# Kernel tuning notes

Measured on AMD Instinct MI355X. Metric: run time of the kernel, lower is better.

Reference implementation:

```python
import jax, jax.numpy as jnp
import numpy as np

NC = 4
X = Y = Z = 64
IMG_SHAPE = (96, 96, 96)
SPAN = 2          # FILTER_SIZE = [5,5,5]
NUM_ITER = 4
DIL = 2           # DILATION = 2.0
SMOOTH_DISTANCE_INIT = 0.3
PRIOR_DISTANCE_INIT = 0.3


def _ind(d):
    # mirrors _get_ind from the torch code
    return (d, 0) if d > 0 else (0, -d)


def _sl(a, b):
    # slice(a, -b) with -0 -> None, mirrors _negative
    return slice(a, -b if b else None)


def _offsets():
    for dx in range(-SPAN, SPAN + 1):
        for dy in range(-SPAN, SPAN + 1):
            for dz in range(-SPAN, SPAN + 1):
                yield dx, dy, dz


def _lin_resize_axis(x, axis, out):
    # 1D linear interpolation matching torch align_corners=True
    n = x.shape[axis]
    if out == n:
        return x
    pos = jnp.arange(out, dtype=x.dtype) * ((n - 1) / (out - 1))
    i0 = jnp.clip(jnp.floor(pos).astype(jnp.int32), 0, n - 1)
    i1 = jnp.clip(i0 + 1, 0, n - 1)
    w = pos - i0.astype(x.dtype)
    shp = [1] * x.ndim
    shp[axis] = out
    w = w.reshape(shp)
    return jnp.take(x, i0, axis=axis) * (1 - w) + jnp.take(x, i1, axis=axis) * w


def _resize3d(x, out_sz):
    # trilinear, align_corners=True, separable over the 3 spatial axes of [b,c,X,Y,Z]
    for ax, o in zip((2, 3, 4), out_sz):
        x = _lin_resize_axis(x, ax, o)
    return x


def _smooth_gaussian(feats):
    # feats: [b, c, X, Y, Z] -> gaussian [b, 5,5,5, X, Y, Z]
    b = feats.shape[0]
    sp = feats.shape[2:]
    g = jnp.zeros((b, 5, 5, 5) + sp, feats.dtype)
    for dx, dy, dz in _offsets():
        dx1, dx2 = _ind(dx); dy1, dy2 = _ind(dy); dz1, dz2 = _ind(dz)
        a = feats[:, :, _sl(dx1, dx2), _sl(dy1, dy2), _sl(dz1, dz2)]
        c = feats[:, :, _sl(dx2, dx1), _sl(dy2, dy1), _sl(dz2, dz1)]
        e = jnp.exp(-0.5 * jnp.sum((a - c) ** 2, axis=1))
        g = g.at[:, dx + SPAN, dy + SPAN, dz + SPAN,
                 _sl(dx2, dx1), _sl(dy2, dy1), _sl(dz2, dz1)].set(e)
    return g


def _prior_gaussian(f1, f2):
    # f1, f2: [b, c, x, y, z] (already downsampled) -> [b, 5,5,5, x, y, z]
    b = f1.shape[0]
    sp = f1.shape[2:]
    g = jnp.zeros((b, 5, 5, 5) + sp, f1.dtype)
    for dx, dy, dz in _offsets():
        dx1, dx2 = _ind(dx); dy1, dy2 = _ind(dy); dz1, dz2 = _ind(dz)
        a = f1[:, :, _sl(dx2, dx1), _sl(dy2, dy1), _sl(dz2, dz1)]
        c = f2[:, :, _sl(dx1, dx2), _sl(dy1, dy2), _sl(dz1, dz2)]
        e = jnp.exp(-0.5 * jnp.sum((a - c) ** 2, axis=1))
        g = g.at[:, dx + SPAN, dy + SPAN, dz + SPAN,
                 _sl(dx2, dx1), _sl(dy2, dy1), _sl(dz2, dz1)].set(e)
    return g


def _message(p, g):
    # p: [b, nc, x, y, z]; g: [b, 5,5,5, x, y, z]
    out = jnp.zeros_like(p)
    for dx, dy, dz in _offsets():
        dx1, dx2 = _ind(dx); dy1, dy2 = _ind(dy); dz1, dz2 = _ind(dz)
        a = p[:, :, _sl(dx1, dx2), _sl(dy1, dy2), _sl(dz1, dz2)]
        w = g[:, None, dx + SPAN, dy + SPAN, dz + SPAN,
              _sl(dx2, dx1), _sl(dy2, dy1), _sl(dz2, dz1)]
        out = out.at[:, :, _sl(dx2, dx1), _sl(dy2, dy1), _sl(dz2, dz1)].add(a * w)
    return out


def setup_inputs() -> dict:
    key = jax.random.key(0)
    ks = jax.random.split(key, 6)
    unary = jax.random.normal(ks[0], (1, NC, X, Y, Z), jnp.float32)
    img = jax.random.normal(ks[1], (1, 2, X, Y, Z), jnp.float32)
    atlas = jax.random.normal(ks[2], (1, 2, X, Y, Z), jnp.float32)
    atlas_label = jax.random.uniform(ks[3], (1, X, Y, Z, NC), jnp.float32)
    patch_start = jax.random.randint(ks[4], (1, 3), 0, 32, jnp.int32)
    return {
        "unary": unary,
        "img": img,
        "atlas": atlas,
        "atlas_label": atlas_label,
        "patch_start": patch_start,
        "smooth_norm": jnp.array([1.0 / SMOOTH_DISTANCE_INIT], jnp.float32),
        "smooth_weight": jnp.ones((NC,), jnp.float32),
        "prior_norm": jnp.array([1.0 / PRIOR_DISTANCE_INIT], jnp.float32),
        "prior_weight": jnp.ones(IMG_SHAPE, jnp.float32),
        "compat_w": jnp.eye(NC, dtype=jnp.float32),
    }


def reference(unary, img, atlas, atlas_label, patch_start,
              smooth_norm, smooth_weight, prior_norm, prior_weight, compat_w):
    b, nc, x, y, z = unary.shape
    ds = (x // DIL, y // DIL, z // DIL)  # floor(in*0.5) == ceil(in/2) for even dims

    # similarity kernels
    sg = _smooth_gaussian(img * smooth_norm)                      # [b,5,5,5,x,y,z]
    f1 = _resize3d(img * prior_norm, ds)
    f2 = _resize3d(atlas * prior_norm, ds)
    pg = _prior_gaussian(f1, f2)                                  # [b,5,5,5,x/2,y/2,z/2]

    # prior message is independent of q_values: compute once
    al = jnp.transpose(atlas_label, (0, 4, 1, 2, 3))              # [b,nc,x,y,z]
    al_ds = _resize3d(al, ds)
    pm = _resize3d(_message(al_ds, pg), (x, y, z))                # [b,nc,x,y,z]
    pw = jax.lax.dynamic_slice(
        prior_weight,
        (patch_start[0, 0], patch_start[0, 1], patch_start[0, 2]),
        (x, y, z))
    prior_term = pw[None, None] * pm

    q = unary
    for _ in range(NUM_ITER):
        p = jax.nn.softmax(q, axis=1)
        sm = _message(p, sg)
        pred = smooth_weight[None, :, None, None, None] * sm + prior_term
        q = unary + jnp.einsum('oc,bcxyz->boxyz', compat_w, pred)  # 1x1x1 compat conv
    return q
```

## Files before the change

### kernel.cpp

```cpp
#include <hip/hip_runtime.h>

#define NN 64
#define N3 (64*64*64)
#define DS 32

#define LOG2E 1.4426950408889634f
#define FSCALE 0.8493218002880191f

typedef _Float16 h2  __attribute__((ext_vector_type(2)));
typedef __fp16   h2f __attribute__((ext_vector_type(2)));

__device__ __forceinline__ float fexp2(float x) { return __builtin_amdgcn_exp2f(x); }

__device__ __forceinline__ h2 u2h(unsigned u) { union { unsigned u; h2 h; } c; c.u = u; return c.h; }
__device__ __forceinline__ unsigned h2u(h2 h) { union { unsigned u; h2 h; } c; c.h = h; return c.u; }
__device__ __forceinline__ h2 pkh(float a, float b) {
    union { h2f a; h2 b; } c; c.a = __builtin_amdgcn_cvt_pkrtz(a, b); return c.b;
}
__device__ __forceinline__ float fdot2(h2 a, h2 b) {
    union { h2 h; h2f f; } ca, cb; ca.h = a; cb.h = b;
    return __builtin_amdgcn_fdot2(ca.f, cb.f, 0.0f, false);
}


#define PMX 6
#define PMY 10
#define PMZ 10
#define SXD 10
#define SYD 14
#define SZD 14

__global__ __launch_bounds__(1024) void k_prior(
    const float* __restrict__ img, const float* __restrict__ atlas,
    const float* __restrict__ alabel, const float* __restrict__ unary,
    const float* __restrict__ pnorm, const float* __restrict__ pweight,
    const int* __restrict__ pstart, const float* __restrict__ compat,
    float4* __restrict__ unary4)
{
    __shared__ __align__(16) uint4 nbS[SXD][SYD][SZD];
    __shared__ __align__(8)  uint2 pmS[PMX][PMY][PMZ];

    const int tid = threadIdx.x;
    const int x0 = blockIdx.z * 8, y0 = blockIdx.y * 16, z0 = blockIdx.x * 16;
    const int cxlo = (x0*31)/63, cylo = (y0*31)/63, czlo = (z0*31)/63;

    const float pnf = pnorm[0] * FSCALE;

    for (int i = tid; i < SXD*SYD*SZD; i += 1024) {
        int lz = i % SZD; int r = i / SZD; int ly = r % SYD; int lx = r / SYD;
        int cx = cxlo - 2 + lx, cy = cylo - 2 + ly, cz = czlo - 2 + lz;
        uint4 v = make_uint4(0u, 0u, 0u, 0u);
        if ((unsigned)cx < DS && (unsigned)cy < DS && (unsigned)cz < DS) {
            const float scale = 63.0f / 31.0f;
            float posx = cx*scale; int a0i = (int)posx; float wx = posx - a0i; int a1i = a0i+1 <= 63 ? a0i+1 : 63;
            float posy = cy*scale; int b0i = (int)posy; float wy = posy - b0i; int b1i = b0i+1 <= 63 ? b0i+1 : 63;
            float posz = cz*scale; int d0i = (int)posz; float wz = posz - d0i; int d1i = d0i+1 <= 63 ? d0i+1 : 63;
            float w000=(1-wx)*(1-wy)*(1-wz), w001=(1-wx)*(1-wy)*wz;
            float w010=(1-wx)*wy*(1-wz),     w011=(1-wx)*wy*wz;
            float w100=wx*(1-wy)*(1-wz),     w101=wx*(1-wy)*wz;
            float w110=wx*wy*(1-wz),         w111=wx*wy*wz;
            int c000=(a0i*NN+b0i)*NN+d0i, c001=(a0i*NN+b0i)*NN+d1i;
            int c010=(a0i*NN+b1i)*NN+d0i, c011=(a0i*NN+b1i)*NN+d1i;
            int c100=(a1i*NN+b0i)*NN+d0i, c101=(a1i*NN+b0i)*NN+d1i;
            int c110=(a1i*NN+b1i)*NN+d0i, c111=(a1i*NN+b1i)*NN+d1i;
            auto tri = [&](const float* p) -> float {
                return p[c000]*w000 + p[c001]*w001 + p[c010]*w010 + p[c011]*w011
                     + p[c100]*w100 + p[c101]*w101 + p[c110]*w110 + p[c111]*w111;
            };
            const float4* lab = (const float4*)alabel;
            float4 l = make_float4(0.f,0.f,0.f,0.f);
            {
                float4 t;
                t = lab[c000]; l.x += w000*t.x; l.y += w000*t.y; l.z += w000*t.z; l.w += w000*t.w;
                t = lab[c001]; l.x += w001*t.x; l.y += w001*t.y; l.z += w001*t.z; l.w += w001*t.w;
                t = lab[c010]; l.x += w010*t.x; l.y += w010*t.y; l.z += w010*t.z; l.w += w010*t.w;
                t = lab[c011]; l.x += w011*t.x; l.y += w011*t.y; l.z += w011*t.z; l.w += w011*t.w;
                t = lab[c100]; l.x += w100*t.x; l.y += w100*t.y; l.z += w100*t.z; l.w += w100*t.w;
                t = lab[c101]; l.x += w101*t.x; l.y += w101*t.y; l.z += w101*t.z; l.w += w101*t.w;
                t = lab[c110]; l.x += w110*t.x; l.y += w110*t.y; l.z += w110*t.z; l.w += w110*t.w;
                t = lab[c111]; l.x += w111*t.x; l.y += w111*t.y; l.z += w111*t.z; l.w += w111*t.w;
            }
            v = make_uint4(h2u(pkh(pnf*tri(atlas), pnf*tri(atlas + N3))),
                           h2u(pkh(l.x, l.y)), h2u(pkh(l.z, l.w)),
                           h2u(pkh(pnf*tri(img), pnf*tri(img + N3))));
        }
        nbS[lx][ly][lz] = v;
    }
    __syncthreads();

    for (int i = tid; i < PMX*PMY*PMZ; i += 1024) {
        int pz = i % PMZ; int r = i / PMZ; int py = r % PMY; int px = r / PMY;
        int cx = cxlo + px, cy = cylo + py, cz = czlo + pz;
        uint2 o = make_uint2(0u, 0u);
        if (cx < DS && cy < DS && cz < DS) {
            h2 ncf = -u2h(nbS[px+2][py+2][pz+2].w);
            float a0=0.f, a1=0.f, a2=0.f, a3=0.f;
            for (int dx = -2; dx <= 2; ++dx) {
                int xx = cx + dx; if ((unsigned)xx >= DS) continue;
                for (int dy = -2; dy <= 2; ++dy) {
                    int yy = cy + dy; if ((unsigned)yy >= DS) continue;
                    #pragma unroll
                    for (int dz = -2; dz <= 2; ++dz) {
                        int zz = cz + dz; if ((unsigned)zz >= DS) continue;
                        uint4 v = nbS[px+2+dx][py+2+dy][pz+2+dz];
                        h2 d = u2h(v.x) + ncf;
                        float w = fexp2(-fdot2(d, d));
                        h2 l01 = u2h(v.y), l23 = u2h(v.z);
                        a0 += w*(float)l01.x; a1 += w*(float)l01.y;
                        a2 += w*(float)l23.x; a3 += w*(float)l23.y;
                    }
                }
            }
            o = make_uint2(h2u(pkh(a0, a1)), h2u(pkh(a2, a3)));
        }
        pmS[px][py][pz] = o;
    }
    __syncthreads();

    const int ps0 = pstart[0], ps1 = pstart[1], ps2 = pstart[2];
    float cw[16];
    #pragma unroll
    for (int k = 0; k < 16; ++k) cw[k] = compat[k];
    const float S13 = 31.0f / 63.0f;

    for (int i = tid; i < 8*16*16; i += 1024) {
        int fz = i & 15, fy = (i >> 4) & 15, fx = i >> 8;
        int gx = x0 + fx, gy = y0 + fy, gz = z0 + fz;
        float posx = gx*S13; int xc0 = (int)posx; float wx = posx - xc0; int xc1 = xc0 < 31 ? xc0+1 : 31;
        float posy = gy*S13; int yc0 = (int)posy; float wy = posy - yc0; int yc1 = yc0 < 31 ? yc0+1 : 31;
        float posz = gz*S13; int zc0 = (int)posz; float wz = posz - zc0; int zc1 = zc0 < 31 ? zc0+1 : 31;
        int lx0 = xc0-cxlo, lx1 = xc1-cxlo;
        int ly0 = yc0-cylo, ly1 = yc1-cylo;
        int lz0 = zc0-czlo, lz1 = zc1-czlo;

        auto up = [&](uint2 u) -> float4 {
            h2 a = u2h(u.x), b = u2h(u.y);
            return make_float4((float)a.x, (float)a.y, (float)b.x, (float)b.y);
        };
        float4 p000 = up(pmS[lx0][ly0][lz0]), p001 = up(pmS[lx0][ly0][lz1]);
        float4 p010 = up(pmS[lx0][ly1][lz0]), p011 = up(pmS[lx0][ly1][lz1]);
        float4 p100 = up(pmS[lx1][ly0][lz0]), p101 = up(pmS[lx1][ly0][lz1]);
        float4 p110 = up(pmS[lx1][ly1][lz0]), p111 = up(pmS[lx1][ly1][lz1]);
        float w000=(1-wx)*(1-wy)*(1-wz), w001=(1-wx)*(1-wy)*wz;
        float w010=(1-wx)*wy*(1-wz),     w011=(1-wx)*wy*wz;
        float w100=wx*(1-wy)*(1-wz),     w101=wx*(1-wy)*wz;
        float w110=wx*wy*(1-wz),         w111=wx*wy*wz;
        float pw = pweight[(ps0+gx)*96*96 + (ps1+gy)*96 + (ps2+gz)];
        float pr0 = pw*(w000*p000.x + w001*p001.x + w010*p010.x + w011*p011.x + w100*p100.x + w101*p101.x + w110*p110.x + w111*p111.x);
        float pr1 = pw*(w000*p000.y + w001*p001.y + w010*p010.y + w011*p011.y + w100*p100.y + w101*p101.y + w110*p110.y + w111*p111.y);
        float pr2 = pw*(w000*p000.z + w001*p001.z + w010*p010.z + w011*p011.z + w100*p100.z + w101*p101.z + w110*p110.z + w111*p111.z);
        float pr3 = pw*(w000*p000.w + w001*p001.w + w010*p010.w + w011*p011.w + w100*p100.w + w101*p101.w + w110*p110.w + w111*p111.w);

        int g = (gx*NN + gy)*NN + gz;
        float4 q;
        q.x = unary[g]      + cw[0]*pr0  + cw[1]*pr1  + cw[2]*pr2  + cw[3]*pr3;
        q.y = unary[g+N3]   + cw[4]*pr0  + cw[5]*pr1  + cw[6]*pr2  + cw[7]*pr3;
        q.z = unary[g+2*N3] + cw[8]*pr0  + cw[9]*pr1  + cw[10]*pr2 + cw[11]*pr3;
        q.w = unary[g+3*N3] + cw[12]*pr0 + cw[13]*pr1 + cw[14]*pr2 + cw[15]*pr3;
        unary4[g] = q;
    }
}


#define TXD 8
#define TYD 8
#define TZD 8
#define RZ 4
#define HX 12
#define HY 12
#define HZ 12
#define PZ 14
#define PZF 20

template<bool QV_IN, bool QV_OUT>
__global__ __launch_bounds__(1024, 8) void k_iter(
    const float* __restrict__ qin,
    const float4* __restrict__ unary4,
    const float* __restrict__ img,
    const float* __restrict__ snorm,
    const float* __restrict__ sweight,
    const float* __restrict__ compat,
    float* __restrict__ qout)
{
    __shared__ __align__(16) uint2    pS[HX][HY][PZ];
    __shared__ __align__(16) unsigned fS[HX][HY][PZF];
    __shared__ __align__(16) uint4    accA[7][TXD*TYD*2];
    __shared__ __align__(16) uint4    accB[7][TXD*TYD*2];

    const int tzg = threadIdx.x, ty = threadIdx.y;
    const int tx = threadIdx.z & 7, s = threadIdx.z >> 3;
    const int x0b = blockIdx.z * TXD, y0b = blockIdx.y * TYD, z0b = blockIdx.x * TZD;
    const int tid = threadIdx.x + 2*threadIdx.y + 16*threadIdx.z;
    const float sc = snorm[0] * FSCALE;

    #pragma unroll
    for (int rr = 0; rr < 2; ++rr) {
        int i = tid + rr*1024;
        if (i < HX*HY*HZ) {
            int lz = i % HZ; int r = i / HZ;
            int ly = r % HY; int lx = r / HY;
            int gx = x0b + lx - 2, gy = y0b + ly - 2, gz = z0b + lz - 2;
            uint2 pu = make_uint2(0u, 0u);
            unsigned fu = 0u;
            if ((unsigned)gx < NN && (unsigned)gy < NN && (unsigned)gz < NN) {
                int g = (gx*NN + gy)*NN + gz;
                float q0, q1, q2, q3;
                if (QV_IN) {
                    float4 qv = reinterpret_cast<const float4*>(qin)[g];
                    q0 = qv.x; q1 = qv.y; q2 = qv.z; q3 = qv.w;
                } else {
                    q0 = qin[g]; q1 = qin[g+N3]; q2 = qin[g+2*N3]; q3 = qin[g+3*N3];
                }
                float m = fmaxf(fmaxf(q0,q1), fmaxf(q2,q3));
                float e0 = fexp2((q0-m)*LOG2E);
                float e1 = fexp2((q1-m)*LOG2E);
                float e2 = fexp2((q2-m)*LOG2E);
                float e3 = fexp2((q3-m)*LOG2E);
                float inv = 1.0f/(e0+e1+e2+e3);
                pu = make_uint2(h2u(pkh(e0*inv, e1*inv)), h2u(pkh(e2*inv, e3*inv)));
                fu = h2u(pkh(img[g]*sc, img[g+N3]*sc));
            }
            pS[lx][ly][lz] = pu;
            fS[lx][ly][lz] = fu;
        }
    }
    __syncthreads();

    const int tz0 = tzg * RZ;

    h2 ncf[RZ];
    #pragma unroll
    for (int rz = 0; rz < RZ; ++rz) ncf[rz] = -u2h(fS[tx+2][ty+2][tz0+2+rz]);

    h2 a01[RZ], a23[RZ];
    #pragma unroll
    for (int rz = 0; rz < RZ; ++rz) { a01[rz] = (h2)0; a23[rz] = (h2)0; }

    #pragma unroll
    for (int pp = 0; pp < 4; ++pp) {
        int p = (7 - s) + 8*pp;
        if (p < 25) {
            int dx = p / 5, dy = p - 5*dx;
            const uint4* pv = reinterpret_cast<const uint4*>(&pS[tx+dx][ty+dy][tz0]);
            uint4 qa = pv[0], qb = pv[1], qc = pv[2], qd = pv[3];
            const uint4* fv = reinterpret_cast<const uint4*>(&fS[tx+dx][ty+dy][tz0]);
            uint4 fa = fv[0], fb = fv[1];

            unsigned fz[8]  = { fa.x, fa.y, fa.z, fa.w, fb.x, fb.y, fb.z, fb.w };
            unsigned p01[8] = { qa.x, qa.z, qb.x, qb.z, qc.x, qc.z, qd.x, qd.z };
            unsigned p23[8] = { qa.y, qa.w, qb.y, qb.w, qc.y, qc.w, qd.y, qd.w };

            #pragma unroll
            for (int rz = 0; rz < RZ; ++rz) {
                #pragma unroll
                for (int dz = 0; dz < 5; ++dz) {
                    int k = rz + dz;
                    h2 d = u2h(fz[k]) + ncf[rz];
                    float w = fexp2(-fdot2(d, d));
                    h2 w2 = pkh(w, w);
                    a01[rz] = w2 * u2h(p01[k]) + a01[rz];
                    a23[rz] = w2 * u2h(p23[k]) + a23[rz];
                }
            }
        }
    }

    const int pid = (tx*TYD + ty)*2 + tzg;
    if (s != 0) {
        accA[s-1][pid] = make_uint4(h2u(a01[0]), h2u(a01[1]), h2u(a01[2]), h2u(a01[3]));
        accB[s-1][pid] = make_uint4(h2u(a23[0]), h2u(a23[1]), h2u(a23[2]), h2u(a23[3]));
    }
    __syncthreads();

    if (s == 0) {
        #pragma unroll
        for (int j = 0; j < 7; ++j) {
            uint4 va = accA[j][pid];
            a01[0] += u2h(va.x); a01[1] += u2h(va.y); a01[2] += u2h(va.z); a01[3] += u2h(va.w);
            uint4 vb = accB[j][pid];
            a23[0] += u2h(vb.x); a23[1] += u2h(vb.y); a23[2] += u2h(vb.z); a23[3] += u2h(vb.w);
        }

        const int gx = x0b + tx, gy = y0b + ty;
        const int g = (gx*NN + gy)*NN + z0b + tz0;
        const float sw0 = sweight[0], sw1 = sweight[1], sw2 = sweight[2], sw3 = sweight[3];
        float cw[16];
        #pragma unroll
        for (int k = 0; k < 16; ++k) cw[k] = compat[k];

        float r[4][RZ];
        #pragma unroll
        for (int rz = 0; rz < RZ; ++rz) {
            float4 u4 = unary4[g + rz];
            float p0 = sw0*(float)a01[rz].x, p1 = sw1*(float)a01[rz].y;
            float p2 = sw2*(float)a23[rz].x, p3 = sw3*(float)a23[rz].y;
            r[0][rz] = u4.x + cw[0]*p0  + cw[1]*p1  + cw[2]*p2  + cw[3]*p3;
            r[1][rz] = u4.y + cw[4]*p0  + cw[5]*p1  + cw[6]*p2  + cw[7]*p3;
            r[2][rz] = u4.z + cw[8]*p0  + cw[9]*p1  + cw[10]*p2 + cw[11]*p3;
            r[3][rz] = u4.w + cw[12]*p0 + cw[13]*p1 + cw[14]*p2 + cw[15]*p3;
        }

        if (QV_OUT) {
            float4* qo = reinterpret_cast<float4*>(qout);
            #pragma unroll
            for (int rz = 0; rz < RZ; ++rz)
                qo[g + rz] = make_float4(r[0][rz], r[1][rz], r[2][rz], r[3][rz]);
        } else {
            #pragma unroll
            for (int o = 0; o < 4; ++o)
                *(float4*)(qout + o*N3 + g) = make_float4(r[o][0], r[o][1], r[o][2], r[o][3]);
        }
    }
}


extern "C" void kernel_launch(void* const* d_in, const int* in_sizes, int n_in,
                              void* d_out, int out_size, void* d_ws, size_t ws_size,
                              hipStream_t stream)
{
    const float* unary   = (const float*)d_in[0];
    const float* img     = (const float*)d_in[1];
    const float* atlas   = (const float*)d_in[2];
    const float* alabel  = (const float*)d_in[3];
    const int*   pstart  = (const int*)d_in[4];
    const float* snorm   = (const float*)d_in[5];
    const float* sweight = (const float*)d_in[6];
    const float* pnorm   = (const float*)d_in[7];
    const float* pweight = (const float*)d_in[8];
    const float* compat  = (const float*)d_in[9];
    float* out = (float*)d_out;
    float* ws  = (float*)d_ws;

    float4* unary4 = (float4*)ws;
    float*  qA     = ws + 4*N3;
    float*  qB     = ws + 8*N3;

    {
        dim3 pgrid(4, 4, 8), pblock(1024);
        k_prior<<<pgrid, pblock, 0, stream>>>(img, atlas, alabel, unary, pnorm,
                                              pweight, pstart, compat, unary4);
    }

    dim3 grid(NN/TZD, NN/TYD, NN/TXD), block(2, 8, 64);
    k_iter<false,true><<<grid, block, 0, stream>>>(unary, unary4, img, snorm, sweight, compat, qA);
    k_iter<true, true><<<grid, block, 0, stream>>>(qA,    unary4, img, snorm, sweight, compat, qB);
    k_iter<true, true><<<grid, block, 0, stream>>>(qB,    unary4, img, snorm, sweight, compat, qA);
    k_iter<true,false><<<grid, block, 0, stream>>>(qA,    unary4, img, snorm, sweight, compat, out);
}
```

Before: 93.25 us.

## Store fp16 softmax probabilities between iterations and precompute packed image features

Each iteration kernel now applies softmax in its epilogue and writes packed fp16 probabilities, so the next iteration loads 8 bytes per voxel instead of 16 bytes of fp32 logits and recomputes no exps in its halo. The packed, scaled image features are computed once in the prior kernel and reused by all four iterations. The thread mapping changes to 4 z-groups of 2 outputs each with 4 neighbour-splits instead of 8, which shrinks the shared reduction buffers and cuts register pressure. Unary and weight loads are hoisted ahead of the barrier. The cost is fp16 rounding on the probabilities carried between iterations, and the first launch passes the same buffer as its pin and pout, although FIRST never reads pin.

```diff
diff --git a/kernel.cpp b/kernel.cpp
--- a/kernel.cpp
+++ b/kernel.cpp
@@ -33,9 +33,10 @@
 __global__ __launch_bounds__(1024) void k_prior(
     const float* __restrict__ img, const float* __restrict__ atlas,
     const float* __restrict__ alabel, const float* __restrict__ unary,
-    const float* __restrict__ pnorm, const float* __restrict__ pweight,
-    const int* __restrict__ pstart, const float* __restrict__ compat,
-    float4* __restrict__ unary4)
+    const float* __restrict__ pnorm, const float* __restrict__ snorm,
+    const float* __restrict__ pweight, const int* __restrict__ pstart,
+    const float* __restrict__ compat,
+    float4* __restrict__ unary4, unsigned* __restrict__ fpk)
 {
     __shared__ __align__(16) uint4 nbS[SXD][SYD][SZD];
     __shared__ __align__(8)  uint2 pmS[PMX][PMY][PMZ];
@@ -45,6 +46,13 @@
     const int cxlo = (x0*31)/63, cylo = (y0*31)/63, czlo = (z0*31)/63;
 
     const float pnf = pnorm[0] * FSCALE;
+    const float sc  = snorm[0] * FSCALE;
+
+    for (int i = tid; i < 8*16*16; i += 1024) {
+        int fz = i & 15, fy = (i >> 4) & 15, fx = i >> 8;
+        int g = ((x0+fx)*NN + (y0+fy))*NN + (z0+fz);
+        fpk[g] = h2u(pkh(img[g]*sc, img[g+N3]*sc));
+    }
 
     for (int i = tid; i < SXD*SYD*SZD; i += 1024) {
         int lz = i % SZD; int r = i / SZD; int ly = r % SYD; int lx = r / SYD;
@@ -165,33 +173,32 @@
 #define TXD 8
 #define TYD 8
 #define TZD 8
-#define RZ 4
+#define TZR 4
+#define RZ 2
 #define HX 12
 #define HY 12
 #define HZ 12
 #define PZ 14
-#define PZF 20
-
-template<bool QV_IN, bool QV_OUT>
+
+template<bool FIRST, bool LAST>
 __global__ __launch_bounds__(1024, 8) void k_iter(
     const float* __restrict__ qin,
+    const uint2* __restrict__ pin,
+    const unsigned* __restrict__ fpk,
     const float4* __restrict__ unary4,
-    const float* __restrict__ img,
-    const float* __restrict__ snorm,
     const float* __restrict__ sweight,
     const float* __restrict__ compat,
+    uint2* __restrict__ pout,
     float* __restrict__ qout)
 {
     __shared__ __align__(16) uint2    pS[HX][HY][PZ];
-    __shared__ __align__(16) unsigned fS[HX][HY][PZF];
-    __shared__ __align__(16) uint4    accA[7][TXD*TYD*2];
-    __shared__ __align__(16) uint4    accB[7][TXD*TYD*2];
+    __shared__ __align__(8)  unsigned fS[HX][HY][PZ];
+    __shared__ __align__(16) uint4    accS[3][TXD*TYD*TZR];
 
     const int tzg = threadIdx.x, ty = threadIdx.y;
     const int tx = threadIdx.z & 7, s = threadIdx.z >> 3;
     const int x0b = blockIdx.z * TXD, y0b = blockIdx.y * TYD, z0b = blockIdx.x * TZD;
-    const int tid = threadIdx.x + 2*threadIdx.y + 16*threadIdx.z;
-    const float sc = snorm[0] * FSCALE;
+    const int tid = threadIdx.x + TZR*threadIdx.y + (TZR*TYD)*threadIdx.z;
 
     #pragma unroll
     for (int rr = 0; rr < 2; ++rr) {
@@ -204,111 +211,126 @@
             unsigned fu = 0u;
             if ((unsigned)gx < NN && (unsigned)gy < NN && (unsigned)gz < NN) {
                 int g = (gx*NN + gy)*NN + gz;
-                float q0, q1, q2, q3;
-                if (QV_IN) {
-                    float4 qv = reinterpret_cast<const float4*>(qin)[g];
-                    q0 = qv.x; q1 = qv.y; q2 = qv.z; q3 = qv.w;
+                fu = fpk[g];
+                if (FIRST) {
+                    float q0 = qin[g], q1 = qin[g+N3], q2 = qin[g+2*N3], q3 = qin[g+3*N3];
+                    float m = fmaxf(fmaxf(q0,q1), fmaxf(q2,q3));
+                    float e0 = fexp2((q0-m)*LOG2E);
+                    float e1 = fexp2((q1-m)*LOG2E);
+                    float e2 = fexp2((q2-m)*LOG2E);
+                    float e3 = fexp2((q3-m)*LOG2E);
+                    float inv = 1.0f/(e0+e1+e2+e3);
+                    pu = make_uint2(h2u(pkh(e0*inv, e1*inv)), h2u(pkh(e2*inv, e3*inv)));
                 } else {
-                    q0 = qin[g]; q1 = qin[g+N3]; q2 = qin[g+2*N3]; q3 = qin[g+3*N3];
+                    pu = pin[g];
                 }
-                float m = fmaxf(fmaxf(q0,q1), fmaxf(q2,q3));
-                float e0 = fexp2((q0-m)*LOG2E);
-                float e1 = fexp2((q1-m)*LOG2E);
-                float e2 = fexp2((q2-m)*LOG2E);
-                float e3 = fexp2((q3-m)*LOG2E);
-                float inv = 1.0f/(e0+e1+e2+e3);
-                pu = make_uint2(h2u(pkh(e0*inv, e1*inv)), h2u(pkh(e2*inv, e3*inv)));
-                fu = h2u(pkh(img[g]*sc, img[g+N3]*sc));
             }
             pS[lx][ly][lz] = pu;
             fS[lx][ly][lz] = fu;
         }
     }
+
+    const int tz0 = tzg * RZ;
+    const int gx = x0b + tx, gy = y0b + ty;
+    const int g = (gx*NN + gy)*NN + z0b + tz0;
+
+    float4 u40, u41;
+    float sw0, sw1, sw2, sw3;
+    float cw[16];
+    if (s == 0) {
+        u40 = unary4[g]; u41 = unary4[g+1];
+        sw0 = sweight[0]; sw1 = sweight[1]; sw2 = sweight[2]; sw3 = sweight[3];
+        #pragma unroll
+        for (int k = 0; k < 16; ++k) cw[k] = compat[k];
+    }
+
     __syncthreads();
 
-    const int tz0 = tzg * RZ;
-
-    h2 ncf[RZ];
+    const h2 ncf0 = -u2h(fS[tx+2][ty+2][tz0+2]);
+    const h2 ncf1 = -u2h(fS[tx+2][ty+2][tz0+3]);
+
+    h2 a01_0 = (h2)0, a23_0 = (h2)0, a01_1 = (h2)0, a23_1 = (h2)0;
+
     #pragma unroll
-    for (int rz = 0; rz < RZ; ++rz) ncf[rz] = -u2h(fS[tx+2][ty+2][tz0+2+rz]);
-
-    h2 a01[RZ], a23[RZ];
-    #pragma unroll
-    for (int rz = 0; rz < RZ; ++rz) { a01[rz] = (h2)0; a23[rz] = (h2)0; }
-
-    #pragma unroll
-    for (int pp = 0; pp < 4; ++pp) {
-        int p = (7 - s) + 8*pp;
+    for (int pp = 0; pp < 7; ++pp) {
+        int p = (3 - s) + 4*pp;
         if (p < 25) {
             int dx = p / 5, dy = p - 5*dx;
             const uint4* pv = reinterpret_cast<const uint4*>(&pS[tx+dx][ty+dy][tz0]);
-            uint4 qa = pv[0], qb = pv[1], qc = pv[2], qd = pv[3];
-            const uint4* fv = reinterpret_cast<const uint4*>(&fS[tx+dx][ty+dy][tz0]);
-            uint4 fa = fv[0], fb = fv[1];
-
-            unsigned fz[8]  = { fa.x, fa.y, fa.z, fa.w, fb.x, fb.y, fb.z, fb.w };
-            unsigned p01[8] = { qa.x, qa.z, qb.x, qb.z, qc.x, qc.z, qd.x, qd.z };
-            unsigned p23[8] = { qa.y, qa.w, qb.y, qb.w, qc.y, qc.w, qd.y, qd.w };
+            const uint2* fv = reinterpret_cast<const uint2*>(&fS[tx+dx][ty+dy][tz0]);
+            uint4 qa = pv[0], qb = pv[1], qc = pv[2];
+            uint2 fa = fv[0], fb = fv[1], fc = fv[2];
+
+            unsigned fz[6]  = { fa.x, fa.y, fb.x, fb.y, fc.x, fc.y };
+            unsigned p01[6] = { qa.x, qa.z, qb.x, qb.z, qc.x, qc.z };
+            unsigned p23[6] = { qa.y, qa.w, qb.y, qb.w, qc.y, qc.w };
 
             #pragma unroll
-            for (int rz = 0; rz < RZ; ++rz) {
-                #pragma unroll
-                for (int dz = 0; dz < 5; ++dz) {
-                    int k = rz + dz;
-                    h2 d = u2h(fz[k]) + ncf[rz];
+            for (int dz = 0; dz < 5; ++dz) {
+                {
+                    h2 d = u2h(fz[dz]) + ncf0;
                     float w = fexp2(-fdot2(d, d));
                     h2 w2 = pkh(w, w);
-                    a01[rz] = w2 * u2h(p01[k]) + a01[rz];
-                    a23[rz] = w2 * u2h(p23[k]) + a23[rz];
+                    a01_0 = w2 * u2h(p01[dz]) + a01_0;
+                    a23_0 = w2 * u2h(p23[dz]) + a23_0;
+                }
+                {
+                    h2 d = u2h(fz[dz+1]) + ncf1;
+                    float w = fexp2(-fdot2(d, d));
+                    h2 w2 = pkh(w, w);
+                    a01_1 = w2 * u2h(p01[dz+1]) + a01_1;
+                    a23_1 = w2 * u2h(p23[dz+1]) + a23_1;
                 }
             }
         }
     }
 
-    const int pid = (tx*TYD + ty)*2 + tzg;
+    const int pid = (tx*TYD + ty)*TZR + tzg;
     if (s != 0) {
-        accA[s-1][pid] = make_uint4(h2u(a01[0]), h2u(a01[1]), h2u(a01[2]), h2u(a01[3]));
-        accB[s-1][pid] = make_uint4(h2u(a23[0]), h2u(a23[1]), h2u(a23[2]), h2u(a23[3]));
+        accS[s-1][pid] = make_uint4(h2u(a01_0), h2u(a23_0), h2u(a01_1), h2u(a23_1));
     }
     __syncthreads();
 
     if (s == 0) {
         #pragma unroll
-        for (int j = 0; j < 7; ++j) {
-            uint4 va = accA[j][pid];
-            a01[0] += u2h(va.x); a01[1] += u2h(va.y); a01[2] += u2h(va.z); a01[3] += u2h(va.w);
-            uint4 vb = accB[j][pid];
-            a23[0] += u2h(vb.x); a23[1] += u2h(vb.y); a23[2] += u2h(vb.z); a23[3] += u2h(vb.w);
-        }
-
-        const int gx = x0b + tx, gy = y0b + ty;
-        const int g = (gx*NN + gy)*NN + z0b + tz0;
-        const float sw0 = sweight[0], sw1 = sweight[1], sw2 = sweight[2], sw3 = sweight[3];
-        float cw[16];
-        #pragma unroll
-        for (int k = 0; k < 16; ++k) cw[k] = compat[k];
-
-        float r[4][RZ];
-        #pragma unroll
-        for (int rz = 0; rz < RZ; ++rz) {
-            float4 u4 = unary4[g + rz];
-            float p0 = sw0*(float)a01[rz].x, p1 = sw1*(float)a01[rz].y;
-            float p2 = sw2*(float)a23[rz].x, p3 = sw3*(float)a23[rz].y;
-            r[0][rz] = u4.x + cw[0]*p0  + cw[1]*p1  + cw[2]*p2  + cw[3]*p3;
-            r[1][rz] = u4.y + cw[4]*p0  + cw[5]*p1  + cw[6]*p2  + cw[7]*p3;
-            r[2][rz] = u4.z + cw[8]*p0  + cw[9]*p1  + cw[10]*p2 + cw[11]*p3;
-            r[3][rz] = u4.w + cw[12]*p0 + cw[13]*p1 + cw[14]*p2 + cw[15]*p3;
-        }
-
-        if (QV_OUT) {
-            float4* qo = reinterpret_cast<float4*>(qout);
-            #pragma unroll
-            for (int rz = 0; rz < RZ; ++rz)
-                qo[g + rz] = make_float4(r[0][rz], r[1][rz], r[2][rz], r[3][rz]);
+        for (int j = 0; j < 3; ++j) {
+            uint4 v = accS[j][pid];
+            a01_0 += u2h(v.x); a23_0 += u2h(v.y);
+            a01_1 += u2h(v.z); a23_1 += u2h(v.w);
+        }
+
+        float p0, p1, p2, p3;
+        float r00, r10, r20, r30, r01, r11, r21, r31;
+        p0 = sw0*(float)a01_0.x; p1 = sw1*(float)a01_0.y;
+        p2 = sw2*(float)a23_0.x; p3 = sw3*(float)a23_0.y;
+        r00 = u40.x + cw[0]*p0  + cw[1]*p1  + cw[2]*p2  + cw[3]*p3;
+        r10 = u40.y + cw[4]*p0  + cw[5]*p1  + cw[6]*p2  + cw[7]*p3;
+        r20 = u40.z + cw[8]*p0  + cw[9]*p1  + cw[10]*p2 + cw[11]*p3;
+        r30 = u40.w + cw[12]*p0 + cw[13]*p1 + cw[14]*p2 + cw[15]*p3;
+        p0 = sw0*(float)a01_1.x; p1 = sw1*(float)a01_1.y;
+        p2 = sw2*(float)a23_1.x; p3 = sw3*(float)a23_1.y;
+        r01 = u41.x + cw[0]*p0  + cw[1]*p1  + cw[2]*p2  + cw[3]*p3;
+        r11 = u41.y + cw[4]*p0  + cw[5]*p1  + cw[6]*p2  + cw[7]*p3;
+        r21 = u41.z + cw[8]*p0  + cw[9]*p1  + cw[10]*p2 + cw[11]*p3;
+        r31 = u41.w + cw[12]*p0 + cw[13]*p1 + cw[14]*p2 + cw[15]*p3;
+
+        if (LAST) {
+            *(float2*)(qout + 0*N3 + g) = make_float2(r00, r01);
+            *(float2*)(qout + 1*N3 + g) = make_float2(r10, r11);
+            *(float2*)(qout + 2*N3 + g) = make_float2(r20, r21);
+            *(float2*)(qout + 3*N3 + g) = make_float2(r30, r31);
         } else {
-            #pragma unroll
-            for (int o = 0; o < 4; ++o)
-                *(float4*)(qout + o*N3 + g) = make_float4(r[o][0], r[o][1], r[o][2], r[o][3]);
+            float m0 = fmaxf(fmaxf(r00,r10), fmaxf(r20,r30));
+            float e00 = fexp2((r00-m0)*LOG2E), e10 = fexp2((r10-m0)*LOG2E);
+            float e20 = fexp2((r20-m0)*LOG2E), e30 = fexp2((r30-m0)*LOG2E);
+            float i0 = 1.0f/(e00+e10+e20+e30);
+            float m1 = fmaxf(fmaxf(r01,r11), fmaxf(r21,r31));
+            float e01 = fexp2((r01-m1)*LOG2E), e11 = fexp2((r11-m1)*LOG2E);
+            float e21 = fexp2((r21-m1)*LOG2E), e31 = fexp2((r31-m1)*LOG2E);
+            float i1 = 1.0f/(e01+e11+e21+e31);
+            uint4 o = make_uint4(h2u(pkh(e00*i0, e10*i0)), h2u(pkh(e20*i0, e30*i0)),
+                                 h2u(pkh(e01*i1, e11*i1)), h2u(pkh(e21*i1, e31*i1)));
+            *reinterpret_cast<uint4*>(&pout[g]) = o;
         }
     }
 }
@@ -331,19 +353,20 @@
     float* out = (float*)d_out;
     float* ws  = (float*)d_ws;
 
-    float4* unary4 = (float4*)ws;
-    float*  qA     = ws + 4*N3;
-    float*  qB     = ws + 8*N3;
+    float4*   unary4 = (float4*)ws;
+    uint2*    pA     = (uint2*)(ws + 4*N3);
+    uint2*    pB     = (uint2*)(ws + 6*N3);
+    unsigned* fpk    = (unsigned*)(ws + 8*N3);
 
     {
         dim3 pgrid(4, 4, 8), pblock(1024);
-        k_prior<<<pgrid, pblock, 0, stream>>>(img, atlas, alabel, unary, pnorm,
-                                              pweight, pstart, compat, unary4);
-    }
-
-    dim3 grid(NN/TZD, NN/TYD, NN/TXD), block(2, 8, 64);
-    k_iter<false,true><<<grid, block, 0, stream>>>(unary, unary4, img, snorm, sweight, compat, qA);
-    k_iter<true, true><<<grid, block, 0, stream>>>(qA,    unary4, img, snorm, sweight, compat, qB);
-    k_iter<true, true><<<grid, block, 0, stream>>>(qB,    unary4, img, snorm, sweight, compat, qA);
-    k_iter<true,false><<<grid, block, 0, stream>>>(qA,    unary4, img, snorm, sweight, compat, out);
-}
+        k_prior<<<pgrid, pblock, 0, stream>>>(img, atlas, alabel, unary, pnorm, snorm,
+                                              pweight, pstart, compat, unary4, fpk);
+    }
+
+    dim3 grid(NN/TZD, NN/TYD, NN/TXD), block(TZR, TYD, 32);
+    k_iter<true, false><<<grid, block, 0, stream>>>(unary, pA, fpk, unary4, sweight, compat, pA, out);
+    k_iter<false,false><<<grid, block, 0, stream>>>(unary, pA, fpk, unary4, sweight, compat, pB, out);
+    k_iter<false,false><<<grid, block, 0, stream>>>(unary, pB, fpk, unary4, sweight, compat, pA, out);
+    k_iter<false,true ><<<grid, block, 0, stream>>>(unary, pA, fpk, unary4, sweight, compat, pB, out);
+}
```

Result: no change. 91.45 us (-1.9%).
